# Kernel tuning notes

Hardware: AMD Instinct MI355X
Metric: run time of the kernel (lower is better)

## Reference

```python
import jax, jax.numpy as jnp
import numpy as np

EMBED_DIM = 1024
NUM_HEADS = 16
HEAD_DIM = EMBED_DIM // NUM_HEADS
SEQ_LEN = 2048
BATCH = 2
THETA_BASE = 10000.0


def rope_angles(head_dim, max_seq_len):
    inv_freq = 1.0 / (THETA_BASE ** (jnp.arange(0, head_dim, 2, dtype=jnp.float32) / head_dim))
    pos = jnp.arange(max_seq_len, dtype=jnp.float32)
    angles = pos[:, None] * inv_freq[None, :]              # [S, D/2]
    angles = jnp.concatenate([angles, angles], axis=-1)    # [S, D]
    return jnp.cos(angles), jnp.sin(angles)


def apply_rope(x, cos, sin):
    # x: [B, H, S, D]; cos/sin: [S, D]
    d = x.shape[-1]
    x1, x2 = x[..., : d // 2], x[..., d // 2 :]
    rotated = jnp.concatenate([-x2, x1], axis=-1)
    return x * cos[None, None, :, :] + rotated * sin[None, None, :, :]


def setup_inputs() -> dict:
    key = jax.random.key(0)
    kx, kq, kk, kv, ko = jax.random.split(key, 5)
    s = 1.0 / np.sqrt(EMBED_DIM)
    return {
        "x": jax.random.normal(kx, (BATCH, SEQ_LEN, EMBED_DIM), dtype=jnp.float32),
        "Wq": jax.random.normal(kq, (EMBED_DIM, EMBED_DIM), dtype=jnp.float32) * s,
        "Wk": jax.random.normal(kk, (EMBED_DIM, EMBED_DIM), dtype=jnp.float32) * s,
        "Wv": jax.random.normal(kv, (EMBED_DIM, EMBED_DIM), dtype=jnp.float32) * s,
        "Wo": jax.random.normal(ko, (EMBED_DIM, EMBED_DIM), dtype=jnp.float32) * s,
    }


def reference(x, Wq, Wk, Wv, Wo):
    B, S, E = x.shape
    H, D = NUM_HEADS, HEAD_DIM
    cos, sin = rope_angles(D, S)

    def split_heads(t):
        return t.reshape(B, S, H, D).transpose(0, 2, 1, 3)  # [B,H,S,D]

    q = split_heads(x @ Wq.T)
    k = split_heads(x @ Wk.T)
    v = split_heads(x @ Wv.T)

    q = apply_rope(q, cos, sin)
    k = apply_rope(k, cos, sin)

    scores = jnp.einsum("bhsd,bhtd->bhst", q, k)
    causal = jnp.triu(jnp.ones((S, S), dtype=bool), k=1)
    scores = jnp.where(causal[None, None, :, :], -jnp.inf, scores)
    weights = jax.nn.softmax(scores / jnp.sqrt(jnp.float32(D)), axis=-1)

    ctx = jnp.einsum("bhst,bhtd->bhsd", weights, v)
    ctx = ctx.transpose(0, 2, 1, 3).reshape(B, S, E)
    return ctx @ Wo.T
```

## Files before the change

kernel.cpp:

```cpp
#include <hip/hip_runtime.h>
#include <hip/hip_bf16.h>

#define H_NUM 16
#define D_DIM 64
#define S_LEN 2048
#define EMB   1024
#define M_TOT 4096

typedef unsigned short u16;
typedef unsigned int   u32;
typedef __attribute__((ext_vector_type(8))) short short8;
typedef __attribute__((ext_vector_type(4))) float f32x4;

__device__ __forceinline__ u32 f2bf_u(float f) {
    u32 u = __float_as_uint(f);
    return (u + 0x7fffu + ((u >> 16) & 1u)) >> 16;
}
__device__ __forceinline__ u32 pack2(float a, float b) {
    return f2bf_u(a) | (f2bf_u(b) << 16);
}
__device__ __forceinline__ u32 pack2t(float a, float b) {
    return __builtin_amdgcn_perm(__float_as_uint(b), __float_as_uint(a),
                                 0x07060302u);
}
__device__ __forceinline__ uint4 pack8(float4 lo, float4 hi) {
    return make_uint4(pack2(lo.x, lo.y), pack2(lo.z, lo.w),
                      pack2(hi.x, hi.y), pack2(hi.z, hi.w));
}

__device__ __forceinline__ void lds_dma16(const u16* g, u16* l) {
    __builtin_amdgcn_global_load_lds(
        (const __attribute__((address_space(1))) void*)g,
        (__attribute__((address_space(3))) void*)l, 16, 0, 0);
}

__global__ __launch_bounds__(256) void cast_kernel(
    const float* __restrict__ x,  const float* __restrict__ Wq,
    const float* __restrict__ Wk, const float* __restrict__ Wv,
    const float* __restrict__ Wo, u16* __restrict__ ws, float2* __restrict__ tab)
{
    const int seg = blockIdx.y;
    if (seg == 5) {
        const int idx = blockIdx.x * 256 + threadIdx.x;
        if (idx < S_LEN * 32) {
            const int s = idx >> 5, d = idx & 31;
            const float ang = (float)s * __expf(-(float)d * 0.28782313662425573f);
            tab[idx] = make_float2(cosf(ang), sinf(ang));
        }
        return;
    }
    const float* src = (seg == 0) ? x : (seg == 1) ? Wq : (seg == 2) ? Wk
                     : (seg == 3) ? Wv : Wo;
    u16* dst = (seg == 0) ? ws : ws + (3 + seg) * 1048576;
    const int n = (seg == 0) ? 4194304 : 1048576;
    const int idx = (blockIdx.x * 256 + threadIdx.x) * 8;
    if (idx < n) {
        float4 lo = *(const float4*)(src + idx);
        float4 hi = *(const float4*)(src + idx + 4);
        *(uint4*)(dst + idx) = pack8(lo, hi);
    }
}

__global__ __launch_bounds__(256) void qkv_rope_kernel(
    const u16* __restrict__ xb, const u16* __restrict__ wb,
    const float2* __restrict__ tab,
    u16* __restrict__ qo, u16* __restrict__ ko, u16* __restrict__ vo)
{
    const int w  = blockIdx.y >> 3;
    const int nb = blockIdx.y & 7;
    const u16* W = wb + w * 1048576;

    __shared__ __align__(16) u16 smem[12288];
    u16* As = smem;
    u16* Bs = smem + 64 * 64;
    u16 (*Ep)[132] = (u16(*)[132])smem;

    const int tid   = threadIdx.x;
    const int lane  = tid & 63;
    const int wid   = tid >> 6;
    const int waveM = wid >> 1;
    const int waveN = wid & 1;
    const int col16 = lane & 15;
    const int quad  = lane >> 4;

    const int m0 = blockIdx.x * 64;
    const int n0 = nb * 128;

    f32x4 acc[2][4];
    const f32x4 zero4 = {0.f, 0.f, 0.f, 0.f};
#pragma unroll
    for (int i = 0; i < 2; i++)
#pragma unroll
        for (int j = 0; j < 4; j++) acc[i][j] = zero4;

    const int drow = tid >> 3;
    const int dpos = tid & 7;
    const u16* Ag = xb + (size_t)m0 * EMB;
    const u16* Bg = W  + (size_t)n0 * EMB;

    for (int k0 = 0; k0 < EMB; k0 += 64) {
        __syncthreads();
#pragma unroll
        for (int j = 0; j < 2; j++) {
            const int rl = j * 32 + drow;
            const int cg = dpos ^ (rl & 7);
            lds_dma16(Ag + (size_t)rl * EMB + k0 + cg * 8,
                      As + (j * 32 + wid * 8) * 64);
        }
#pragma unroll
        for (int j = 0; j < 4; j++) {
            const int rl = j * 32 + drow;
            const int cg = dpos ^ (rl & 7);
            lds_dma16(Bg + (size_t)rl * EMB + k0 + cg * 8,
                      Bs + (j * 32 + wid * 8) * 64);
        }
        __syncthreads();

        short8 af[2][2], bf[4][2];
#pragma unroll
        for (int mt = 0; mt < 2; mt++) {
            const int r = waveM * 32 + mt * 16 + col16;
#pragma unroll
            for (int ks = 0; ks < 2; ks++) {
                const int p = (ks * 4 + quad) ^ (r & 7);
                af[mt][ks] = *(const short8*)(As + r * 64 + p * 8);
            }
        }
#pragma unroll
        for (int nt = 0; nt < 4; nt++) {
            const int r = waveN * 64 + nt * 16 + col16;
#pragma unroll
            for (int ks = 0; ks < 2; ks++) {
                const int p = (ks * 4 + quad) ^ (r & 7);
                bf[nt][ks] = *(const short8*)(Bs + r * 64 + p * 8);
            }
        }
#pragma unroll
        for (int ks = 0; ks < 2; ks++)
#pragma unroll
            for (int mt = 0; mt < 2; mt++)
#pragma unroll
                for (int nt = 0; nt < 4; nt++)
                    acc[mt][nt] = __builtin_amdgcn_mfma_f32_16x16x32_bf16(
                        af[mt][ks], bf[nt][ks], acc[mt][nt], 0, 0, 0);
    }

    __syncthreads();
#pragma unroll
    for (int mt = 0; mt < 2; mt++) {
#pragma unroll
        for (int r = 0; r < 4; r++) {
            const int m_local = waveM * 32 + mt * 16 + quad * 4 + r;
            const int s = (m0 + m_local) & 2047;
            if (w == 2) {
#pragma unroll
                for (int nt = 0; nt < 4; nt++)
                    Ep[m_local][waveN * 64 + nt * 16 + col16] =
                        (u16)f2bf_u(acc[mt][nt][r]);
            } else {
#pragma unroll
                for (int nt = 0; nt < 2; nt++) {
                    const int d = nt * 16 + col16;
                    const float2 cs = tab[s * 32 + d];
                    const float lo = acc[mt][nt][r];
                    const float hi = acc[mt][nt + 2][r];
                    Ep[m_local][waveN * 64 + d]      = (u16)f2bf_u(lo * cs.x - hi * cs.y);
                    Ep[m_local][waveN * 64 + d + 32] = (u16)f2bf_u(hi * cs.x + lo * cs.y);
                }
            }
        }
    }
    __syncthreads();

    const int b = m0 >> 11;
    if (w != 2) {
        u16* out = (w == 0) ? qo : ko;
#pragma unroll
        for (int j = 0; j < 4; j++) {
            const int g = j * 256 + tid;
            const int head_local = g >> 9;
            const int sl  = (g >> 3) & 63;
            const int cir = g & 7;
            uint4 val = *(const uint4*)(&Ep[sl][head_local * 64 + cir * 8]);
            const int h = (n0 >> 6) + head_local;
            const size_t base = (((size_t)(b * H_NUM + h)) * S_LEN + (m0 & 2047)) * 64;
            *(uint4*)(out + base + (size_t)(g & 511) * 8) = val;
        }
    } else {
        const int s0 = m0 & 2047;
#pragma unroll
        for (int j = 0; j < 4; j++) {
            const int g = j * 256 + tid;
            const int d_all = g >> 3;
            const int sc = g & 7;
            u32 wv[4];
#pragma unroll
            for (int hw = 0; hw < 4; hw++) {
                const int p0 = sc * 8 + hw * 2;
                const int r0 = ((p0 & 3) << 4) | (p0 >> 2);
                const int p1 = p0 + 1;
                const int r1 = ((p1 & 3) << 4) | (p1 >> 2);
                wv[hw] = (u32)Ep[r0][d_all] | ((u32)Ep[r1][d_all] << 16);
            }
            const int h = (n0 >> 6) + (d_all >> 6);
            const int d = d_all & 63;
            *(uint4*)(vo + ((size_t)(b * H_NUM + h) * 64 + d) * 2048 + s0 + sc * 8) =
                make_uint4(wv[0], wv[1], wv[2], wv[3]);
        }
    }
}

__global__ __launch_bounds__(256) void attn_kernel(
    const u16* __restrict__ q, const u16* __restrict__ k,
    const u16* __restrict__ v, u16* __restrict__ ctx)
{
    __shared__ __align__(16) u16 QP[64 * 64];
    __shared__ __align__(16) u16 Ks[2][64 * 64];
    __shared__ __align__(16) u16 VTs[2][64 * 64];

    const int tid   = threadIdx.x;
    const int lane  = tid & 63;
    const int wid   = tid >> 6;
    const int col16 = lane & 15;
    const int quad  = lane >> 4;

    const int bh = blockIdx.x;
    const int y = blockIdx.y;
    const int o = y & 7, g = y >> 3;
    const int qb = (g == 0) ? (31 - o) : (g == 1) ? (16 + o)
                 : (g == 2) ? (15 - o) : o;
    const int qBase = qb * 64;
    const size_t bhOff = (size_t)bh * S_LEN * D_DIM;

    const int drow = tid >> 3;
    const int dpos = tid & 7;

    auto stage = [&](int kt, int buf) {
#pragma unroll
        for (int j = 0; j < 2; j++) {
            const int rl = j * 32 + drow;
            const int cg = dpos ^ (rl & 7);
            lds_dma16(k + bhOff + (size_t)(kt * 64 + rl) * 64 + cg * 8,
                      &Ks[buf][(j * 32 + wid * 8) * 64]);
        }
#pragma unroll
        for (int j = 0; j < 2; j++) {
            const int rl = j * 32 + drow;
            const int cg = dpos ^ (rl & 7);
            lds_dma16(v + bhOff + (size_t)rl * 2048 + kt * 64 + cg * 8,
                      &VTs[buf][(j * 32 + wid * 8) * 64]);
        }
    };

    stage(0, 0);
#pragma unroll
    for (int j = 0; j < 2; j++) {
        const int rl = j * 32 + drow;
        const int cg = dpos ^ (rl & 7);
        lds_dma16(q + bhOff + (size_t)(qBase + rl) * 64 + cg * 8,
                  QP + (j * 32 + wid * 8) * 64);
    }
    __syncthreads();

    short8 qf[2];
    {
        const int rq = wid * 16 + col16;
#pragma unroll
        for (int ks = 0; ks < 2; ks++) {
            const int c = (ks * 4 + quad) ^ (rq & 7);
            qf[ks] = *(const short8*)(QP + rq * 64 + c * 8);
        }
    }

    f32x4 O[4];
    const f32x4 zero4 = {0.f, 0.f, 0.f, 0.f};
#pragma unroll
    for (int j = 0; j < 4; j++) O[j] = zero4;
    float lrun[4] = {0.f, 0.f, 0.f, 0.f};

    const float K2 = 0.18033688011112042f;

    for (int kt = 0; kt <= qb; kt++) {
        if (kt > 0) __syncthreads();
        if (kt < qb) stage(kt + 1, (kt + 1) & 1);
        const int cur = kt & 1;

        f32x4 sc[4];
#pragma unroll
        for (int nt = 0; nt < 4; nt++) sc[nt] = zero4;
#pragma unroll
        for (int ks = 0; ks < 2; ks++) {
            short8 kf[4];
#pragma unroll
            for (int nt = 0; nt < 4; nt++) {
                const int rk = nt * 16 + col16;
                const int c = (ks * 4 + quad) ^ (rk & 7);
                kf[nt] = *(const short8*)(&Ks[cur][rk * 64 + c * 8]);
            }
#pragma unroll
            for (int nt = 0; nt < 4; nt++)
                sc[nt] = __builtin_amdgcn_mfma_f32_16x16x32_bf16(
                    qf[ks], kf[nt], sc[nt], 0, 0, 0);
        }

        if (kt == qb) {
#pragma unroll
            for (int r = 0; r < 4; r++) {
                const int qg = qBase + wid * 16 + quad * 4 + r;
                float lsum = 0.f;
#pragma unroll
                for (int nt = 0; nt < 4; nt++) {
                    const int kg = kt * 64 + nt * 16 + col16;
                    float sv = fmaf(sc[nt][r], K2, -16.0f);
                    if (kg > qg) sv = -INFINITY;
                    const float p = exp2f(sv);
                    sc[nt][r] = p;
                    lsum += p;
                }
                lrun[r] += lsum;
            }
        } else {
#pragma unroll
            for (int r = 0; r < 4; r++) {
                float lsum = 0.f;
#pragma unroll
                for (int nt = 0; nt < 4; nt++) {
                    const float p = exp2f(fmaf(sc[nt][r], K2, -16.0f));
                    sc[nt][r] = p;
                    lsum += p;
                }
                lrun[r] += lsum;
            }
        }

#pragma unroll
        for (int r = 0; r < 4; r++) {
            const int ml = quad * 4 + r;
            const u32 lo = pack2t(sc[0][r], sc[1][r]);
            const u32 hi = pack2t(sc[2][r], sc[3][r]);
            *(uint2*)(QP + (wid * 16 + ml) * 64 +
                      (((col16 >> 1) ^ (ml & 7)) * 8 + (col16 & 1) * 4)) =
                make_uint2(lo, hi);
        }

#pragma unroll
        for (int ks = 0; ks < 2; ks++) {
            short8 pf, vf[4];
            {
                const int c = (ks * 4 + quad) ^ (col16 & 7);
                pf = *(const short8*)(QP + (wid * 16 + col16) * 64 + c * 8);
            }
#pragma unroll
            for (int dt = 0; dt < 4; dt++) {
                const int d = dt * 16 + col16;
                const int c = (ks * 4 + quad) ^ (d & 7);
                vf[dt] = *(const short8*)(&VTs[cur][d * 64 + c * 8]);
            }
#pragma unroll
            for (int dt = 0; dt < 4; dt++)
                O[dt] = __builtin_amdgcn_mfma_f32_16x16x32_bf16(
                    pf, vf[dt], O[dt], 0, 0, 0);
        }
    }

#pragma unroll
    for (int r = 0; r < 4; r++) {
#pragma unroll
        for (int o2 = 1; o2 < 16; o2 <<= 1)
            lrun[r] += __shfl_xor(lrun[r], o2);
    }

    const int b = bh >> 4, h = bh & 15;
#pragma unroll
    for (int r = 0; r < 4; r++) {
        const int ml = quad * 4 + r;
        const float inv = 1.0f / lrun[r];
        const u32 lo = pack2t(O[0][r] * inv, O[1][r] * inv);
        const u32 hi = pack2t(O[2][r] * inv, O[3][r] * inv);
        *(uint2*)(QP + (wid * 16 + ml) * 64 +
                  (((col16 >> 1) ^ (ml & 7)) * 8 + (col16 & 1) * 4)) =
            make_uint2(lo, hi);
    }
#pragma unroll
    for (int j = 0; j < 2; j++) {
        const int gg  = j * 64 + lane;
        const int sl = gg >> 3;
        const int cir = gg & 7;
        u32 wv[4];
#pragma unroll
        for (int hw = 0; hw < 4; hw++) {
            const int d0 = cir * 8 + hw * 2;
            const int p0 = ((d0 & 15) << 2) | (d0 >> 4);
            const int d1 = d0 + 1;
            const int p1 = ((d1 & 15) << 2) | (d1 >> 4);
            const u16 v0 = QP[(wid * 16 + sl) * 64 + ((p0 >> 3) ^ (sl & 7)) * 8 + (p0 & 7)];
            const u16 v1 = QP[(wid * 16 + sl) * 64 + ((p1 >> 3) ^ (sl & 7)) * 8 + (p1 & 7)];
            wv[hw] = (u32)v0 | ((u32)v1 << 16);
        }
        const size_t rowbase =
            ((size_t)b * S_LEN + qBase + wid * 16 + sl) * EMB + h * 64;
        *(uint4*)(ctx + rowbase + cir * 8) = make_uint4(wv[0], wv[1], wv[2], wv[3]);
    }
}

__global__ __launch_bounds__(256) void proj_kernel(
    const u16* __restrict__ X, const u16* __restrict__ W, float* __restrict__ out)
{
    __shared__ __align__(16) u16 smem[8192];
    u16* As = smem;
    u16* Bs = smem + 64 * 64;

    const int tid   = threadIdx.x;
    const int lane  = tid & 63;
    const int wid   = tid >> 6;
    const int col16 = lane & 15;
    const int quad  = lane >> 4;

    const int m0 = blockIdx.x * 64;
    const int n0 = blockIdx.y * 64;

    f32x4 acc[4];
    const f32x4 zero4 = {0.f, 0.f, 0.f, 0.f};
#pragma unroll
    for (int i = 0; i < 4; i++) acc[i] = zero4;

    const int drow = tid >> 3;
    const int dpos = tid & 7;
    const u16* Ag = X + (size_t)m0 * EMB;
    const u16* Bg = W + (size_t)n0 * EMB;

    for (int k0 = 0; k0 < EMB; k0 += 64) {
        __syncthreads();
#pragma unroll
        for (int j = 0; j < 2; j++) {
            const int rl = j * 32 + drow;
            const int cg = dpos ^ (rl & 7);
            lds_dma16(Ag + (size_t)rl * EMB + k0 + cg * 8,
                      As + (j * 32 + wid * 8) * 64);
        }
#pragma unroll
        for (int j = 0; j < 2; j++) {
            const int rl = j * 32 + drow;
            const int cg = dpos ^ (rl & 7);
            lds_dma16(Bg + (size_t)rl * EMB + k0 + cg * 8,
                      Bs + (j * 32 + wid * 8) * 64);
        }
        __syncthreads();

        short8 af[2], bf[4][2];
        {
            const int r = wid * 16 + col16;
#pragma unroll
            for (int ks = 0; ks < 2; ks++) {
                const int p = (ks * 4 + quad) ^ (r & 7);
                af[ks] = *(const short8*)(As + r * 64 + p * 8);
            }
        }
#pragma unroll
        for (int nt = 0; nt < 4; nt++) {
            const int r = nt * 16 + col16;
#pragma unroll
            for (int ks = 0; ks < 2; ks++) {
                const int p = (ks * 4 + quad) ^ (r & 7);
                bf[nt][ks] = *(const short8*)(Bs + r * 64 + p * 8);
            }
        }
#pragma unroll
        for (int ks = 0; ks < 2; ks++)
#pragma unroll
            for (int nt = 0; nt < 4; nt++)
                acc[nt] = __builtin_amdgcn_mfma_f32_16x16x32_bf16(
                    bf[nt][ks], af[ks], acc[nt], 0, 0, 0);
    }

#pragma unroll
    for (int nt = 0; nt < 4; nt++) {
        const int m_g = m0 + wid * 16 + col16;
        const int n_g = n0 + nt * 16 + quad * 4;
        *(f32x4*)(out + (size_t)m_g * EMB + n_g) = acc[nt];
    }
}

extern "C" void kernel_launch(void* const* d_in, const int* in_sizes, int n_in,
                              void* d_out, int out_size, void* d_ws, size_t ws_size,
                              hipStream_t stream)
{
    const float* x  = (const float*)d_in[0];
    const float* Wq = (const float*)d_in[1];
    const float* Wk = (const float*)d_in[2];
    const float* Wv = (const float*)d_in[3];
    const float* Wo = (const float*)d_in[4];

    u16* ws = (u16*)d_ws;
    u16* xb  = ws;
    u16* wb  = ws + 4194304;
    u16* wob = ws + 7340032;
    u16* q   = ws + 8388608;
    u16* k   = ws + 12582912;
    u16* v   = ws + 16777216;
    u16* ctx = ws + 20971520;
    float2* tab = (float2*)(ws + 25165824);

    cast_kernel<<<dim3(2048, 6), 256, 0, stream>>>(x, Wq, Wk, Wv, Wo, ws, tab);
    qkv_rope_kernel<<<dim3(64, 24), 256, 0, stream>>>(xb, wb, tab, q, k, v);
    attn_kernel<<<dim3(32, 32), 256, 0, stream>>>(q, k, v, ctx);
    proj_kernel<<<dim3(64, 16), 256, 0, stream>>>(ctx, wob, (float*)d_out);
}
```

Before: 171.3 us.

## Fold softmax scale into Q projection and compute row sums via MFMA

The softmax scale (1/sqrt(D)*log2e) is folded into the Q epilogue of the projection kernel, so the attention loop applies exp2 directly to the scores. The fixed -16 offset is dropped, which risks overflow for large logits. Per-row sums are now accumulated with an extra MFMA against a ones vector on the bf16-rounded P, replacing the scalar adds and the final cross-lane shuffles. s_setprio is also raised around the MFMA groups to favour matrix issue between waves.

```diff
diff --git a/kernel.cpp b/kernel.cpp
--- a/kernel.cpp
+++ b/kernel.cpp
@@ -145,6 +145,7 @@
                         af[mt][ks], bf[nt][ks], acc[mt][nt], 0, 0, 0);
     }
 
+    const float qs = (w == 0) ? 0.18033688011112042f : 1.0f;
     __syncthreads();
 #pragma unroll
     for (int mt = 0; mt < 2; mt++) {
@@ -164,8 +165,10 @@
                     const float2 cs = tab[s * 32 + d];
                     const float lo = acc[mt][nt][r];
                     const float hi = acc[mt][nt + 2][r];
-                    Ep[m_local][waveN * 64 + d]      = (u16)f2bf_u(lo * cs.x - hi * cs.y);
-                    Ep[m_local][waveN * 64 + d + 32] = (u16)f2bf_u(hi * cs.x + lo * cs.y);
+                    Ep[m_local][waveN * 64 + d]      =
+                        (u16)f2bf_u((lo * cs.x - hi * cs.y) * qs);
+                    Ep[m_local][waveN * 64 + d + 32] =
+                        (u16)f2bf_u((hi * cs.x + lo * cs.y) * qs);
                 }
             }
         }
@@ -272,13 +275,14 @@
         }
     }
 
+    const short ONE = (short)0x3F80;
+    const short8 onesf = {ONE, ONE, ONE, ONE, ONE, ONE, ONE, ONE};
+
     f32x4 O[4];
     const f32x4 zero4 = {0.f, 0.f, 0.f, 0.f};
 #pragma unroll
     for (int j = 0; j < 4; j++) O[j] = zero4;
-    float lrun[4] = {0.f, 0.f, 0.f, 0.f};
-
-    const float K2 = 0.18033688011112042f;
+    f32x4 lacc = zero4;
 
     for (int kt = 0; kt <= qb; kt++) {
         if (kt > 0) __syncthreads();
@@ -297,39 +301,32 @@
                 const int c = (ks * 4 + quad) ^ (rk & 7);
                 kf[nt] = *(const short8*)(&Ks[cur][rk * 64 + c * 8]);
             }
+            __builtin_amdgcn_s_setprio(1);
 #pragma unroll
             for (int nt = 0; nt < 4; nt++)
                 sc[nt] = __builtin_amdgcn_mfma_f32_16x16x32_bf16(
                     qf[ks], kf[nt], sc[nt], 0, 0, 0);
+            __builtin_amdgcn_s_setprio(0);
         }
 
         if (kt == qb) {
 #pragma unroll
             for (int r = 0; r < 4; r++) {
                 const int qg = qBase + wid * 16 + quad * 4 + r;
-                float lsum = 0.f;
 #pragma unroll
                 for (int nt = 0; nt < 4; nt++) {
                     const int kg = kt * 64 + nt * 16 + col16;
-                    float sv = fmaf(sc[nt][r], K2, -16.0f);
-                    if (kg > qg) sv = -INFINITY;
-                    const float p = exp2f(sv);
+                    float p = exp2f(sc[nt][r]);
+                    if (kg > qg) p = 0.f;
                     sc[nt][r] = p;
-                    lsum += p;
                 }
-                lrun[r] += lsum;
             }
         } else {
 #pragma unroll
             for (int r = 0; r < 4; r++) {
-                float lsum = 0.f;
-#pragma unroll
-                for (int nt = 0; nt < 4; nt++) {
-                    const float p = exp2f(fmaf(sc[nt][r], K2, -16.0f));
-                    sc[nt][r] = p;
-                    lsum += p;
-                }
-                lrun[r] += lsum;
+#pragma unroll
+                for (int nt = 0; nt < 4; nt++)
+                    sc[nt][r] = exp2f(sc[nt][r]);
             }
         }
 
@@ -356,25 +353,22 @@
                 const int c = (ks * 4 + quad) ^ (d & 7);
                 vf[dt] = *(const short8*)(&VTs[cur][d * 64 + c * 8]);
             }
+            __builtin_amdgcn_s_setprio(1);
 #pragma unroll
             for (int dt = 0; dt < 4; dt++)
                 O[dt] = __builtin_amdgcn_mfma_f32_16x16x32_bf16(
                     pf, vf[dt], O[dt], 0, 0, 0);
-        }
-    }
-
-#pragma unroll
-    for (int r = 0; r < 4; r++) {
-#pragma unroll
-        for (int o2 = 1; o2 < 16; o2 <<= 1)
-            lrun[r] += __shfl_xor(lrun[r], o2);
+            lacc = __builtin_amdgcn_mfma_f32_16x16x32_bf16(
+                pf, onesf, lacc, 0, 0, 0);
+            __builtin_amdgcn_s_setprio(0);
+        }
     }
 
     const int b = bh >> 4, h = bh & 15;
 #pragma unroll
     for (int r = 0; r < 4; r++) {
         const int ml = quad * 4 + r;
-        const float inv = 1.0f / lrun[r];
+        const float inv = 1.0f / lacc[r];
         const u32 lo = pack2t(O[0][r] * inv, O[1][r] * inv);
         const u32 hi = pack2t(O[2][r] * inv, O[3][r] * inv);
         *(uint2*)(QP + (wid * 16 + ml) * 64 +
```

New measurement: 173.8 us. No clear change (+1.5%).
